# Performance work log

Hardware: AMD Instinct MI355X
Metric: run time of the kernel (lower is better)

The kernel has to match this reference:

```python
import jax, jax.numpy as jnp
import numpy as np

N, V, T, C_IN, C_OUT, REL, H4, H5 = 256, 25, 128, 64, 64, 9, 18, 6


def setup_inputs() -> dict:
    key = jax.random.key(0)
    ks = jax.random.split(key, 12)

    def w(k, shape, fan_in):
        return (jax.random.normal(k, shape, jnp.float32) / np.sqrt(fan_in)).astype(jnp.float32)

    return {
        "x": jax.random.normal(ks[0], (N, V, T, C_IN), jnp.float32),
        "A": jax.random.uniform(ks[1], (V, V), dtype=jnp.float32),
        "W1": w(ks[2], (C_IN, REL), C_IN), "b1": jnp.zeros((REL,), jnp.float32),
        "W2": w(ks[3], (C_IN, REL), C_IN), "b2": jnp.zeros((REL,), jnp.float32),
        "W3": w(ks[4], (C_IN, REL), C_IN), "b3": jnp.zeros((REL,), jnp.float32),
        "W4a": w(ks[5], (REL, H4), REL), "b4a": jnp.zeros((H4,), jnp.float32),
        "W4b": w(ks[6], (H4, REL), H4), "b4b": jnp.zeros((REL,), jnp.float32),
        "W5a": w(ks[7], (REL, H5), REL), "b5a": jnp.zeros((H5,), jnp.float32),
        "W5b": w(ks[8], (H5, C_OUT), H5), "b5b": jnp.zeros((C_OUT,), jnp.float32),
    }


def reference(x, A, W1, b1, W2, b2, W3, b3, W4a, b4a, W4b, b4b, W5a, b5a, W5b, b5b):
    silu = jax.nn.silu
    alpha = 1.0
    # x: (N, V, T, C) channels-last; Linear projections to rel channels
    x1 = x @ W1 + b1                       # (N, V, T, R)
    x2 = x @ W2 + b2                       # (N, V, T, R)
    x3 = x @ W3 + b3                       # (N, V, T, R)
    # temporal mean (original: transpose(1,3).mean(-2))
    m1 = x1.mean(axis=2)                   # (N, V, R)
    m2 = x2.mean(axis=2)                   # (N, V, R)
    # pairwise joint affinity via broadcast difference
    rel = m1[:, :, None, :] - m2[:, None, :, :]   # (N, V, V, R)
    # small MLP (Linear4) on channel dim
    h = silu(rel @ W4a + b4a)              # (N, V, V, 18)
    h = silu(h @ W4b + b4b)                # (N, V, V, R)
    # scale + static adjacency (broadcast over batch and channels)
    h = h * alpha + A[None, :, :, None]    # (N, V, V, R)
    # einsum 'ncuv,nctv->nctu' in channels-last form: aggregate over v
    agg = jnp.einsum('nuvc,nvtc->nutc', h, x3)    # (N, V, T, R)
    # output MLP (Linear5)
    y = silu(agg @ W5a + b5a)              # (N, V, T, 6)
    y = silu(y @ W5b + b5b)                # (N, V, T, C_out)
    return y
```

## Files before the change

kernel.cpp:

```cpp
#include <hip/hip_runtime.h>
#include <hip/hip_fp16.h>

#define NN 256
#define VV 25
#define TT 128
#define CIN 64
#define CO 64
#define RR 9
#define HH4 18
#define HH5 6
#define TQ 16
#define NT 8

typedef unsigned int uint;

__device__ __forceinline__ float silu_f(float v) {
  return __fdividef(v, 1.0f + __expf(-v));
}
__device__ __forceinline__ __half2 u2h(uint u) {
  union { uint x; __half2 h; } c; c.x = u; return c.h;
}
__device__ __forceinline__ uint h2u(__half2 h) {
  union { __half2 h; uint x; } c; c.h = h; return c.x;
}

__global__ __launch_bounds__(128) void k1_proj(
    const float* __restrict__ x, const float* __restrict__ W3,
    const float* __restrict__ b3, uint* __restrict__ x3g,
    float* __restrict__ xm) {
  const int blk = blockIdx.x;
  const int n = blk / VV, v = blk - n * VV;
  const int tid = threadIdx.x;
  __shared__ __align__(16) __half xt[TT * 66];
  __shared__ __align__(16) float xmp[2][64];

  const float4* src = (const float4*)(x + (size_t)blk * TT * CIN);
  float4 r[16];
  #pragma unroll
  for (int k = 0; k < 16; ++k) r[k] = src[k * 128 + tid];
  #pragma unroll
  for (int k = 0; k < 16; ++k) {
    const int idx = k * 128 + tid;
    const int t = idx >> 4, c = (idx & 15) * 4;
    *(__half2*)(&xt[t * 66 + c])     = __floats2half2_rn(r[k].x, r[k].y);
    *(__half2*)(&xt[t * 66 + c + 2]) = __floats2half2_rn(r[k].z, r[k].w);
  }
  float4 cs = r[0];
  #pragma unroll
  for (int k = 1; k < 16; ++k) {
    cs.x += r[k].x; cs.y += r[k].y; cs.z += r[k].z; cs.w += r[k].w;
  }
  #pragma unroll
  for (int m = 16; m < 64; m <<= 1) {
    cs.x += __shfl_xor(cs.x, m); cs.y += __shfl_xor(cs.y, m);
    cs.z += __shfl_xor(cs.z, m); cs.w += __shfl_xor(cs.w, m);
  }
  if ((tid & 63) < 16) *(float4*)(&xmp[tid >> 6][(tid & 15) * 4]) = cs;
  __syncthreads();
  if (tid < 64) xm[(size_t)blk * 64 + tid] = xmp[0][tid] + xmp[1][tid];

  float acc[RR];
  #pragma unroll
  for (int j = 0; j < RR; ++j) acc[j] = b3[j];
  const __half* xrow = xt + tid * 66;
  #pragma unroll 8
  for (int c2 = 0; c2 < 32; ++c2) {
    const __half2 hv = *(const __half2*)(&xrow[c2 * 2]);
    const float x0 = __low2float(hv), x1 = __high2float(hv);
    #pragma unroll
    for (int j = 0; j < RR; ++j) {
      acc[j] = fmaf(x0, W3[(c2 * 2 + 0) * RR + j], acc[j]);
      acc[j] = fmaf(x1, W3[(c2 * 2 + 1) * RR + j], acc[j]);
    }
  }
  uint w[5];
  w[0] = h2u(__floats2half2_rn(acc[0], acc[1]));
  w[1] = h2u(__floats2half2_rn(acc[2], acc[3]));
  w[2] = h2u(__floats2half2_rn(acc[4], acc[5]));
  w[3] = h2u(__floats2half2_rn(acc[6], acc[7]));
  w[4] = h2u(__floats2half2_rn(acc[8], 0.f));
  const int tq = tid >> 4, t = tid & 15;
  uint* dst = x3g + (size_t)(n * NT + tq) * (5 * VV * TQ) + v * TQ + t;
  #pragma unroll
  for (int c = 0; c < 5; ++c) dst[c * (VV * TQ)] = w[c];
}

__global__ __launch_bounds__(128) void k2_h(
    const float* __restrict__ xm, const float* __restrict__ A,
    const float* __restrict__ W1, const float* __restrict__ b1,
    const float* __restrict__ W2, const float* __restrict__ b2,
    const float* __restrict__ W4a, const float* __restrict__ b4a,
    const float* __restrict__ W4b, const float* __restrict__ b4b,
    uint* __restrict__ h2g) {
  const int n = blockIdx.x;
  const int tid = threadIdx.x;
  __shared__ float m1[VV][RR + 1];
  __shared__ float m2[VV][RR + 1];
  const float* xmn = xm + (size_t)n * VV * CIN;
  for (int i = tid; i < 2 * VV * RR; i += 128) {
    const int which = (i >= VV * RR);
    const int idx = which ? i - VV * RR : i;
    const int v = idx / RR, c = idx - v * RR;
    const float* W = which ? W2 : W1;
    const float* b = which ? b2 : b1;
    const float* row = xmn + v * CIN;
    float s = 0.f;
    #pragma unroll
    for (int k = 0; k < CIN; ++k) s = fmaf(row[k], W[k * RR + c], s);
    s = s * (1.0f / TT) + b[c];
    if (which) m2[v][c] = s; else m1[v][c] = s;
  }
  __syncthreads();
  for (int p = tid; p < VV * VV; p += 128) {
    const int u = p / VV, v2 = p - u * VV;
    float rel[RR];
    #pragma unroll
    for (int j = 0; j < RR; ++j) rel[j] = m1[u][j] - m2[v2][j];
    float t1[HH4];
    #pragma unroll
    for (int k = 0; k < HH4; ++k) {
      float s = b4a[k];
      #pragma unroll
      for (int j = 0; j < RR; ++j) s = fmaf(rel[j], W4a[j * HH4 + k], s);
      t1[k] = silu_f(s);
    }
    const float av = A[u * VV + v2];
    float hc[RR];
    #pragma unroll
    for (int j = 0; j < RR; ++j) {
      float s = b4b[j];
      #pragma unroll
      for (int k = 0; k < HH4; ++k) s = fmaf(t1[k], W4b[k * RR + j], s);
      hc[j] = silu_f(s) + av;
    }
    uint* hp = h2g + (size_t)n * (VV * VV * 5) + (size_t)p * 5;
    hp[0] = h2u(__floats2half2_rn(hc[0], hc[1]));
    hp[1] = h2u(__floats2half2_rn(hc[2], hc[3]));
    hp[2] = h2u(__floats2half2_rn(hc[4], hc[5]));
    hp[3] = h2u(__floats2half2_rn(hc[6], hc[7]));
    hp[4] = h2u(__floats2half2_rn(hc[8], 0.f));
  }
}

__global__ __launch_bounds__(256) void k3_out(
    const uint* __restrict__ x3g, const uint* __restrict__ h2g,
    const float* __restrict__ W5a, const float* __restrict__ b5a,
    const float* __restrict__ W5b, const float* __restrict__ b5b,
    float* __restrict__ out) {
  const int bid = blockIdx.x;
  const int uh = bid & 1;
  const int tile = bid >> 1;
  const int n = tile >> 3, tq = tile & 7;
  const int u0 = uh ? 13 : 0;
  const int ucnt = uh ? 12 : 13;
  const int tid = threadIdx.x;
  __shared__ __align__(16) uint x3s[5 * VV * TQ];
  __shared__ __align__(16) uint a5s[13 * TQ * 3];

  {
    const uint4* xsrc = (const uint4*)(x3g + (size_t)tile * (5 * VV * TQ));
    for (int i = tid; i < (5 * VV * TQ) / 4; i += 256)
      ((uint4*)x3s)[i] = xsrc[i];
  }
  __syncthreads();

  if (tid < ucnt * TQ) {
    const int ul = tid >> 4, t = tid & 15;
    const int u = u0 + ul;
    const uint* hr = h2g + (size_t)n * (VV * VV * 5) + u * (VV * 5);
    const uint* xr = x3s + t;
    __half2 c0 = u2h(0u), c1 = c0, c2 = c0, c3 = c0, c4 = c0;
    #pragma unroll 5
    for (int v2 = 0; v2 < VV; ++v2) {
      const int xo = v2 * TQ;
      const uint x0 = xr[xo];
      const uint x1 = xr[xo + 400];
      const uint x2 = xr[xo + 800];
      const uint x3 = xr[xo + 1200];
      const uint x4 = xr[xo + 1600];
      const uint* hv = hr + v2 * 5;
      c0 = __hfma2(u2h(hv[0]), u2h(x0), c0);
      c1 = __hfma2(u2h(hv[1]), u2h(x1), c1);
      c2 = __hfma2(u2h(hv[2]), u2h(x2), c2);
      c3 = __hfma2(u2h(hv[3]), u2h(x3), c3);
      c4 = __hfma2(u2h(hv[4]), u2h(x4), c4);
    }
    float ag[RR];
    ag[0] = __low2float(c0); ag[1] = __high2float(c0);
    ag[2] = __low2float(c1); ag[3] = __high2float(c1);
    ag[4] = __low2float(c2); ag[5] = __high2float(c2);
    ag[6] = __low2float(c3); ag[7] = __high2float(c3);
    ag[8] = __low2float(c4);
    float a5v[HH5];
    #pragma unroll
    for (int k = 0; k < HH5; ++k) {
      float s = b5a[k];
      #pragma unroll
      for (int j = 0; j < RR; ++j) s = fmaf(ag[j], W5a[j * HH5 + k], s);
      a5v[k] = silu_f(s);
    }
    a5s[tid * 3 + 0] = h2u(__floats2half2_rn(a5v[0], a5v[1]));
    a5s[tid * 3 + 1] = h2u(__floats2half2_rn(a5v[2], a5v[3]));
    a5s[tid * 3 + 2] = h2u(__floats2half2_rn(a5v[4], a5v[5]));
  }

  const int cq = (tid & 15) * 4;
  float4 wb[HH5];
  #pragma unroll
  for (int k = 0; k < HH5; ++k) wb[k] = *(const float4*)(W5b + k * CO + cq);
  const float4 bb = *(const float4*)(b5b + cq);
  __syncthreads();

  const int trow = tid >> 4;
  for (int it = 0; it < ucnt; ++it) {
    const int q = it * 16 + trow;
    const int u = u0 + it;
    const __half2 p01 = u2h(a5s[q * 3 + 0]);
    const __half2 p23 = u2h(a5s[q * 3 + 1]);
    const __half2 p45 = u2h(a5s[q * 3 + 2]);
    const float a0 = __low2float(p01), a1 = __high2float(p01);
    const float a2 = __low2float(p23), a3 = __high2float(p23);
    const float a4 = __low2float(p45), a5 = __high2float(p45);
    float4 y;
    y.x = silu_f(bb.x + a0 * wb[0].x + a1 * wb[1].x + a2 * wb[2].x +
                 a3 * wb[3].x + a4 * wb[4].x + a5 * wb[5].x);
    y.y = silu_f(bb.y + a0 * wb[0].y + a1 * wb[1].y + a2 * wb[2].y +
                 a3 * wb[3].y + a4 * wb[4].y + a5 * wb[5].y);
    y.z = silu_f(bb.z + a0 * wb[0].z + a1 * wb[1].z + a2 * wb[2].z +
                 a3 * wb[3].z + a4 * wb[4].z + a5 * wb[5].z);
    y.w = silu_f(bb.w + a0 * wb[0].w + a1 * wb[1].w + a2 * wb[2].w +
                 a3 * wb[3].w + a4 * wb[4].w + a5 * wb[5].w);
    float* orow = out +
        ((size_t)(n * VV + u) * TT + tq * TQ + trow) * CO + cq;
    *(float4*)orow = y;
  }
}

extern "C" void kernel_launch(void* const* d_in, const int* in_sizes, int n_in,
                              void* d_out, int out_size, void* d_ws, size_t ws_size,
                              hipStream_t stream) {
  const float* x   = (const float*)d_in[0];
  const float* A   = (const float*)d_in[1];
  const float* W1  = (const float*)d_in[2];
  const float* b1  = (const float*)d_in[3];
  const float* W2  = (const float*)d_in[4];
  const float* b2  = (const float*)d_in[5];
  const float* W3  = (const float*)d_in[6];
  const float* b3  = (const float*)d_in[7];
  const float* W4a = (const float*)d_in[8];
  const float* b4a = (const float*)d_in[9];
  const float* W4b = (const float*)d_in[10];
  const float* b4b = (const float*)d_in[11];
  const float* W5a = (const float*)d_in[12];
  const float* b5a = (const float*)d_in[13];
  const float* W5b = (const float*)d_in[14];
  const float* b5b = (const float*)d_in[15];
  float* out = (float*)d_out;

  char* ws = (char*)d_ws;
  uint*  x3g = (uint*)ws;
  float* xm  = (float*)(ws + 16384000);
  uint*  h2g = (uint*)(ws + 16384000 + 1638400);

  hipLaunchKernelGGL(k1_proj, dim3(NN * VV), dim3(128), 0, stream,
                     x, W3, b3, x3g, xm);
  hipLaunchKernelGGL(k2_h, dim3(NN), dim3(128), 0, stream,
                     xm, A, W1, b1, W2, b2, W4a, b4a, W4b, b4b, h2g);
  hipLaunchKernelGGL(k3_out, dim3(NN * NT * 2), dim3(256), 0, stream,
                     x3g, h2g, W5a, b5a, W5b, b5b, out);
}
```

Baseline: 148.7 us.

## Fuse affinity-MLP kernel into projection kernel via last-block-per-batch atomic counter

The separate k2_h kernel is removed. Its work now runs inside k1_proj, done by whichever of the 25 joint blocks for a batch element finishes last, detected with an atomic counter and thread fences. The aim is to save a kernel launch and to overlap the small per-batch MLP with other batches' projection work. In exchange it adds a memset launch, an atomic per block, and a serial tail on the last block of each batch, and it reuses the xt shared buffer for the means.

```diff
diff --git a/kernel.cpp b/kernel.cpp
--- a/kernel.cpp
+++ b/kernel.cpp
@@ -25,14 +25,21 @@
 }
 
 __global__ __launch_bounds__(128) void k1_proj(
-    const float* __restrict__ x, const float* __restrict__ W3,
-    const float* __restrict__ b3, uint* __restrict__ x3g,
-    float* __restrict__ xm) {
+    const float* __restrict__ x,
+    const float* __restrict__ W1, const float* __restrict__ b1,
+    const float* __restrict__ W2, const float* __restrict__ b2,
+    const float* __restrict__ W3, const float* __restrict__ b3,
+    const float* __restrict__ W4a, const float* __restrict__ b4a,
+    const float* __restrict__ W4b, const float* __restrict__ b4b,
+    const float* __restrict__ A,
+    uint* __restrict__ x3g, float* __restrict__ xm,
+    uint* __restrict__ h2g, int* __restrict__ cnt) {
   const int blk = blockIdx.x;
   const int n = blk / VV, v = blk - n * VV;
   const int tid = threadIdx.x;
   __shared__ __align__(16) __half xt[TT * 66];
   __shared__ __align__(16) float xmp[2][64];
+  __shared__ int eflag;
 
   const float4* src = (const float4*)(x + (size_t)blk * TT * CIN);
   float4 r[16];
@@ -83,62 +90,60 @@
   uint* dst = x3g + (size_t)(n * NT + tq) * (5 * VV * TQ) + v * TQ + t;
   #pragma unroll
   for (int c = 0; c < 5; ++c) dst[c * (VV * TQ)] = w[c];
-}
-
-__global__ __launch_bounds__(128) void k2_h(
-    const float* __restrict__ xm, const float* __restrict__ A,
-    const float* __restrict__ W1, const float* __restrict__ b1,
-    const float* __restrict__ W2, const float* __restrict__ b2,
-    const float* __restrict__ W4a, const float* __restrict__ b4a,
-    const float* __restrict__ W4b, const float* __restrict__ b4b,
-    uint* __restrict__ h2g) {
-  const int n = blockIdx.x;
-  const int tid = threadIdx.x;
-  __shared__ float m1[VV][RR + 1];
-  __shared__ float m2[VV][RR + 1];
-  const float* xmn = xm + (size_t)n * VV * CIN;
-  for (int i = tid; i < 2 * VV * RR; i += 128) {
-    const int which = (i >= VV * RR);
-    const int idx = which ? i - VV * RR : i;
-    const int v = idx / RR, c = idx - v * RR;
-    const float* W = which ? W2 : W1;
-    const float* b = which ? b2 : b1;
-    const float* row = xmn + v * CIN;
-    float s = 0.f;
-    #pragma unroll
-    for (int k = 0; k < CIN; ++k) s = fmaf(row[k], W[k * RR + c], s);
-    s = s * (1.0f / TT) + b[c];
-    if (which) m2[v][c] = s; else m1[v][c] = s;
-  }
-  __syncthreads();
-  for (int p = tid; p < VV * VV; p += 128) {
-    const int u = p / VV, v2 = p - u * VV;
-    float rel[RR];
-    #pragma unroll
-    for (int j = 0; j < RR; ++j) rel[j] = m1[u][j] - m2[v2][j];
-    float t1[HH4];
-    #pragma unroll
-    for (int k = 0; k < HH4; ++k) {
-      float s = b4a[k];
-      #pragma unroll
-      for (int j = 0; j < RR; ++j) s = fmaf(rel[j], W4a[j * HH4 + k], s);
-      t1[k] = silu_f(s);
-    }
-    const float av = A[u * VV + v2];
-    float hc[RR];
-    #pragma unroll
-    for (int j = 0; j < RR; ++j) {
-      float s = b4b[j];
-      #pragma unroll
-      for (int k = 0; k < HH4; ++k) s = fmaf(t1[k], W4b[k * RR + j], s);
-      hc[j] = silu_f(s) + av;
-    }
-    uint* hp = h2g + (size_t)n * (VV * VV * 5) + (size_t)p * 5;
-    hp[0] = h2u(__floats2half2_rn(hc[0], hc[1]));
-    hp[1] = h2u(__floats2half2_rn(hc[2], hc[3]));
-    hp[2] = h2u(__floats2half2_rn(hc[4], hc[5]));
-    hp[3] = h2u(__floats2half2_rn(hc[6], hc[7]));
-    hp[4] = h2u(__floats2half2_rn(hc[8], 0.f));
+
+  __syncthreads();
+  if (tid == 0) {
+    __threadfence();
+    eflag = (atomicAdd(&cnt[n], 1) == VV - 1);
+  }
+  __syncthreads();
+  if (eflag) {
+    __threadfence();
+    float* m12 = (float*)xt;
+    const float* xmn = xm + (size_t)n * VV * CIN;
+    for (int i = tid; i < 2 * VV * RR; i += 128) {
+      const int which = (i >= VV * RR);
+      const int idx = which ? i - VV * RR : i;
+      const int vv = idx / RR, c = idx - vv * RR;
+      const float* W = which ? W2 : W1;
+      const float* b = which ? b2 : b1;
+      const float* row = xmn + vv * CIN;
+      float s = 0.f;
+      #pragma unroll
+      for (int k = 0; k < CIN; ++k) s = fmaf(row[k], W[k * RR + c], s);
+      m12[(which * VV + vv) * 10 + c] = s * (1.0f / TT) + b[c];
+    }
+    __syncthreads();
+    for (int p = tid; p < VV * VV; p += 128) {
+      const int u = p / VV, v2 = p - u * VV;
+      float rel[RR];
+      #pragma unroll
+      for (int j = 0; j < RR; ++j)
+        rel[j] = m12[u * 10 + j] - m12[(VV + v2) * 10 + j];
+      float t1[HH4];
+      #pragma unroll
+      for (int k = 0; k < HH4; ++k) {
+        float s = b4a[k];
+        #pragma unroll
+        for (int j = 0; j < RR; ++j) s = fmaf(rel[j], W4a[j * HH4 + k], s);
+        t1[k] = silu_f(s);
+      }
+      const float av = A[u * VV + v2];
+      float hc[RR];
+      #pragma unroll
+      for (int j = 0; j < RR; ++j) {
+        float s = b4b[j];
+        #pragma unroll
+        for (int k = 0; k < HH4; ++k) s = fmaf(t1[k], W4b[k * RR + j], s);
+        hc[j] = silu_f(s) + av;
+      }
+      uint* hp = h2g + (size_t)n * (VV * VV * 5) + (size_t)p * 5;
+      hp[0] = h2u(__floats2half2_rn(hc[0], hc[1]));
+      hp[1] = h2u(__floats2half2_rn(hc[2], hc[3]));
+      hp[2] = h2u(__floats2half2_rn(hc[4], hc[5]));
+      hp[3] = h2u(__floats2half2_rn(hc[6], hc[7]));
+      hp[4] = h2u(__floats2half2_rn(hc[8], 0.f));
+    }
   }
 }
 
@@ -261,11 +266,12 @@
   uint*  x3g = (uint*)ws;
   float* xm  = (float*)(ws + 16384000);
   uint*  h2g = (uint*)(ws + 16384000 + 1638400);
-
+  int*   cnt = (int*)(ws + 21222400);
+
+  hipMemsetAsync(cnt, 0, NN * sizeof(int), stream);
   hipLaunchKernelGGL(k1_proj, dim3(NN * VV), dim3(128), 0, stream,
-                     x, W3, b3, x3g, xm);
-  hipLaunchKernelGGL(k2_h, dim3(NN), dim3(128), 0, stream,
-                     xm, A, W1, b1, W2, b2, W4a, b4a, W4b, b4b, h2g);
+                     x, W1, b1, W2, b2, W3, b3, W4a, b4a, W4b, b4b, A,
+                     x3g, xm, h2g, cnt);
   hipLaunchKernelGGL(k3_out, dim3(NN * NT * 2), dim3(256), 0, stream,
                      x3g, h2g, W5a, b5a, W5b, b5b, out);
 }
```

Result: slower. 578.1 us (+288.9%).
